# Kernel optimization log

Hardware: AMD Instinct MI355X
Metric: run time of the kernel (lower is better)

The kernel has to match this reference:

```python
import jax, jax.numpy as jnp
import numpy as np

B, T, C, H = 4, 2048, 1024, 16  # batch, seq, embed, heads; head_dim = C // H = 64


def setup_inputs() -> dict:
    key = jax.random.key(0)
    ks = jax.random.split(key, 9)
    s = 1.0 / np.sqrt(C)
    return {
        "query": jax.random.normal(ks[0], (B, T, C), jnp.float32),
        "key": jax.random.normal(ks[1], (B, T, C), jnp.float32),
        "value": jax.random.normal(ks[2], (B, T, C), jnp.float32),
        "mask": jax.random.randint(ks[3], (1, 1, T, T), 0, 2, jnp.int32),
        "Wq": jax.random.normal(ks[4], (C, C), jnp.float32) * s,
        "Wk": jax.random.normal(ks[5], (C, C), jnp.float32) * s,
        "Wv": jax.random.normal(ks[6], (C, C), jnp.float32) * s,
        "Wp": jax.random.normal(ks[7], (C, C), jnp.float32) * s,
        "bp": jax.random.normal(ks[8], (C,), jnp.float32) * s,
    }


def reference(query, key, value, mask, Wq, Wk, Wv, Wp, bp):
    # torch Linear: y = x @ W.T (no bias for q/k/v)
    q = jnp.einsum("btc,dc->btd", query, Wq)
    k = jnp.einsum("btc,dc->btd", key, Wk)
    v = jnp.einsum("btc,dc->btd", value, Wv)
    hd = C // H
    # [B,T,C] -> [B,H,T,hd]
    q = q.reshape(B, T, H, hd).transpose(0, 2, 1, 3)
    k = k.reshape(B, T, H, hd).transpose(0, 2, 1, 3)
    v = v.reshape(B, T, H, hd).transpose(0, 2, 1, 3)
    # NOTE: scale uses FULL embed dim C (faithful to source), not head_dim.
    wei = jnp.einsum("bhqd,bhkd->bhqk", q, k) * (C ** -0.5)
    # Faithful quirk: masked positions are zero-filled (not -inf) BEFORE softmax.
    wei = jnp.where(mask == 0, jnp.zeros((), wei.dtype), wei)
    wei = jax.nn.softmax(wei, axis=-1)
    out = jnp.einsum("bhqk,bhkd->bhqd", wei, v)
    out = out.transpose(0, 2, 1, 3).reshape(B, T, C)
    # proj (dropout omitted: eval mode / p=0)
    return jnp.einsum("btc,dc->btd", out, Wp) + bp
```

## Files before the change

kernel.cpp:

```cpp
#include <hip/hip_runtime.h>
#include <hip/hip_bf16.h>
#include <cstdint>
#include <cstddef>

static constexpr int Bn = 4, Tn = 2048, Cn = 1024, Hn = 16, HD = 64;
static constexpr int Mn = Bn * Tn;
static constexpr float SCALE = 0.03125f;

typedef __attribute__((ext_vector_type(8))) short s16x8;
typedef __attribute__((ext_vector_type(4))) short s16x4;
typedef __attribute__((ext_vector_type(4))) float f32x4;
typedef __attribute__((ext_vector_type(2))) unsigned u32x2;

#define DEVFN __device__ __forceinline__

DEVFN unsigned short f2bf(float f) {
  union { float f; unsigned u; } v; v.f = f;
  unsigned r = v.u + 0x7fffu + ((v.u >> 16) & 1u);
  return (unsigned short)(r >> 16);
}

DEVFN void gload_lds16(const void* g, void* l) {
  __builtin_amdgcn_global_load_lds(
      (const __attribute__((address_space(1))) void*)g,
      (__attribute__((address_space(3))) void*)l, 16, 0, 0);
}

__global__ __launch_bounds__(256) void k_cvt(const float* __restrict__ in,
                                             unsigned short* __restrict__ out, int n4) {
  int i = blockIdx.x * 256 + threadIdx.x;
  if (i >= n4) return;
  float4 v = reinterpret_cast<const float4*>(in)[i];
  ushort4 o;
  o.x = f2bf(v.x); o.y = f2bf(v.y); o.z = f2bf(v.z); o.w = f2bf(v.w);
  reinterpret_cast<ushort4*>(out)[i] = o;
}

__global__ __launch_bounds__(256) void k_pack(const int* __restrict__ mask,
                                              unsigned* __restrict__ bits) {
  int i = blockIdx.x * 256 + threadIdx.x;
  unsigned long long b = __ballot(mask[i] != 0);
  int lane = threadIdx.x & 63;
  if (lane == 0)        bits[i >> 5] = (unsigned)b;
  else if (lane == 32)  bits[i >> 5] = (unsigned)(b >> 32);
}

template <bool F32OUT>
__global__ __launch_bounds__(256) void k_gemm(const unsigned short* __restrict__ A,
                                              const unsigned short* __restrict__ Bt,
                                              void* __restrict__ Cv,
                                              const float* __restrict__ bias,
                                              float oscale,
                                              int M, int N, int K) {
  __shared__ __align__(16) char As[128 * 64 * 2];
  __shared__ __align__(16) char Bs[128 * 64 * 2];
  const int tid = threadIdx.x, lane = tid & 63, wid = tid >> 6;
  const int l15 = lane & 15, lg = lane >> 4;
  const int wm = (wid >> 1) * 64, wn = (wid & 1) * 64;
  const int m0 = blockIdx.y * 128, n0 = blockIdx.x * 128;

  f32x4 acc[4][4];
#pragma unroll
  for (int i = 0; i < 4; ++i)
#pragma unroll
    for (int j = 0; j < 4; ++j) acc[i][j] = f32x4{0.f, 0.f, 0.f, 0.f};

  for (int k0 = 0; k0 < K; k0 += 64) {
#pragma unroll
    for (int it = 0; it < 4; ++it) {
      int chunk = it * 256 + tid;
      int row = chunk >> 3;
      int kg = (chunk & 7) ^ (row & 7);
      gload_lds16(A + (size_t)(m0 + row) * K + k0 + kg * 8,
                  As + (it * 256 + wid * 64) * 16);
      gload_lds16(Bt + (size_t)(n0 + row) * K + k0 + kg * 8,
                  Bs + (it * 256 + wid * 64) * 16);
    }
    __syncthreads();
#pragma unroll
    for (int kk = 0; kk < 64; kk += 32) {
      s16x8 a[4], b[4];
#pragma unroll
      for (int i = 0; i < 4; ++i) {
        int ra = wm + i * 16 + l15;
        a[i] = *(const s16x8*)(As + ra * 128 + (((kk + lg * 8) * 2) ^ ((ra & 7) << 4)));
        int rb = wn + i * 16 + l15;
        b[i] = *(const s16x8*)(Bs + rb * 128 + (((kk + lg * 8) * 2) ^ ((rb & 7) << 4)));
      }
#pragma unroll
      for (int i = 0; i < 4; ++i)
#pragma unroll
        for (int j = 0; j < 4; ++j)
          acc[i][j] = __builtin_amdgcn_mfma_f32_16x16x32_bf16(a[i], b[j], acc[i][j], 0, 0, 0);
    }
    __syncthreads();
  }
#pragma unroll
  for (int i = 0; i < 4; ++i)
#pragma unroll
    for (int j = 0; j < 4; ++j)
#pragma unroll
      for (int q = 0; q < 4; ++q) {
        int r = m0 + wm + i * 16 + lg * 4 + q;
        int c = n0 + wn + j * 16 + l15;
        float v = acc[i][j][q];
        if (F32OUT) ((float*)Cv)[(size_t)r * N + c] = v + bias[c];
        else        ((unsigned short*)Cv)[(size_t)r * N + c] = f2bf(v * oscale);
      }
}

__global__ __launch_bounds__(256) void k_attn(const unsigned short* __restrict__ Qg,
                                              const unsigned short* __restrict__ Kg,
                                              const unsigned short* __restrict__ Vg,
                                              const unsigned* __restrict__ mbits,
                                              unsigned short* __restrict__ Og) {
  __shared__ __align__(16) char QPs[128 * 128];
  __shared__ __align__(16) char Ks[64 * 128];
  __shared__ __align__(16) char Vts[64 * 128];
  __shared__ unsigned Mw[128 * 2];
  __shared__ float Ls[128];

  const int tid = threadIdx.x, lane = tid & 63, wid = tid >> 6;
  const int l15 = lane & 15, lg = lane >> 4;
  const int qt = blockIdx.x, bh = blockIdx.y;
  const int b = bh >> 4, h = bh & 15;
  const size_t rowbase = (size_t)b * Tn;
  const int cbase = h * 64;

  const int dp = lane & 31;
  const int g  = wid * 2 + (lane >> 5);
  const int qrm = tid >> 1, wmi = tid & 1;

#pragma unroll
  for (int it = 0; it < 4; ++it) {
    int chunk = it * 256 + tid;
    int row = chunk >> 3;
    int kg = (chunk & 7) ^ (row & 7);
    gload_lds16(Qg + (rowbase + qt * 128 + row) * Cn + cbase + kg * 8,
                QPs + (it * 256 + wid * 64) * 16);
  }
#pragma unroll
  for (int it = 0; it < 2; ++it) {
    int chunk = it * 256 + tid;
    int row = chunk >> 3;
    int kg = (chunk & 7) ^ (row & 7);
    gload_lds16(Kg + (rowbase + row) * Cn + cbase + kg * 8,
                Ks + (it * 256 + wid * 64) * 16);
  }
  unsigned w[8];
  {
    const unsigned* vsrc = (const unsigned*)(Vg + (rowbase + g * 8) * Cn + cbase) + dp;
#pragma unroll
    for (int j = 0; j < 8; ++j) w[j] = vsrc[(size_t)j * (Cn / 2)];
  }
  unsigned mreg = mbits[(size_t)(qt * 128 + qrm) * (Tn / 32) + wmi];
  __syncthreads();

  s16x8 qf[2][2];
#pragma unroll
  for (int m = 0; m < 2; ++m)
#pragma unroll
    for (int kh = 0; kh < 2; ++kh) {
      int ra = wid * 32 + m * 16 + l15;
      qf[m][kh] = *(const s16x8*)(QPs + ra * 128 + ((kh * 64 + lg * 16) ^ ((ra & 7) << 4)));
    }
  {
    union { unsigned u[4]; s16x8 v; } lo, hi;
#pragma unroll
    for (int j = 0; j < 4; ++j) {
      lo.u[j] = __builtin_amdgcn_perm(w[2 * j + 1], w[2 * j], 0x05040100u);
      hi.u[j] = __builtin_amdgcn_perm(w[2 * j + 1], w[2 * j], 0x07060302u);
    }
    int d0 = dp * 2, swv = (dp & 7) << 4;
    *(s16x8*)(Vts + d0 * 128 + ((g * 16) ^ swv)) = lo.v;
    *(s16x8*)(Vts + (d0 + 1) * 128 + ((g * 16) ^ swv)) = hi.v;
    Mw[qrm * 2 + wmi] = mreg;
  }

  f32x4 oacc[2][4];
#pragma unroll
  for (int m = 0; m < 2; ++m)
#pragma unroll
    for (int n = 0; n < 4; ++n) oacc[m][n] = f32x4{0.f, 0.f, 0.f, 0.f};
  float lsum[2] = {0.0f, 0.0f};

  char* Pw = QPs + wid * (32 * 128);

  for (int kt = 0; kt < Tn / 64; ++kt) {
    f32x4 sacc[4][2];
#pragma unroll
    for (int n = 0; n < 4; ++n)
#pragma unroll
      for (int m = 0; m < 2; ++m) sacc[n][m] = f32x4{0.f, 0.f, 0.f, 0.f};
#pragma unroll
    for (int kk = 0; kk < 64; kk += 32) {
      s16x8 kfr[4];
#pragma unroll
      for (int n = 0; n < 4; ++n) {
        int rb = n * 16 + l15;
        kfr[n] = *(const s16x8*)(Ks + rb * 128 + (((kk + lg * 8) * 2) ^ ((rb & 7) << 4)));
      }
#pragma unroll
      for (int n = 0; n < 4; ++n)
#pragma unroll
        for (int m = 0; m < 2; ++m)
          sacc[n][m] = __builtin_amdgcn_mfma_f32_16x16x32_bf16(kfr[n], qf[m][kk >> 5],
                                                               sacc[n][m], 0, 0, 0);
    }
    __syncthreads();

    {
      int ktn = (kt + 1) & (Tn / 64 - 1);
#pragma unroll
      for (int it = 0; it < 2; ++it) {
        int chunk = it * 256 + tid;
        int row = chunk >> 3;
        int kg = (chunk & 7) ^ (row & 7);
        gload_lds16(Kg + (rowbase + ktn * 64 + row) * Cn + cbase + kg * 8,
                    Ks + (it * 256 + wid * 64) * 16);
      }
      const unsigned* vsrc =
          (const unsigned*)(Vg + (rowbase + ktn * 64 + g * 8) * Cn + cbase) + dp;
#pragma unroll
      for (int j = 0; j < 8; ++j) w[j] = vsrc[(size_t)j * (Cn / 2)];
      mreg = mbits[(size_t)(qt * 128 + qrm) * (Tn / 32) + ktn * 2 + wmi];
    }

#pragma unroll
    for (int qi = 0; qi < 2; ++qi) {
      int qr = wid * 32 + qi * 16 + l15;
      unsigned w0 = Mw[qr * 2], w1 = Mw[qr * 2 + 1];
      int qloc = qi * 16 + l15;
      unsigned swz = (unsigned)((qloc & 7) << 4);
      float psum = 0.0f;
#pragma unroll
      for (int kf = 0; kf < 4; ++kf) {
        unsigned wm_ = (kf < 2) ? w0 : w1;
        unsigned bits4 = wm_ >> ((kf & 1) * 16 + lg * 4);
        unsigned pb[4];
#pragma unroll
        for (int r = 0; r < 4; ++r) {
          int smear = (int)(bits4 << (31 - r)) >> 31;
          union { float f; unsigned u; } sv; sv.f = sacc[kf][qi][r];
          sv.u &= (unsigned)smear;
          float pv = __expf(sv.f);
          psum += pv;
          union { float f; unsigned u; } pc; pc.f = pv; pb[r] = pc.u;
        }
        union { u32x2 u; s16x4 s; } pk;
        pk.u.x = __builtin_amdgcn_perm(pb[1], pb[0], 0x07060302u);
        pk.u.y = __builtin_amdgcn_perm(pb[3], pb[2], 0x07060302u);
        *(s16x4*)(Pw + qloc * 128 + (((unsigned)(kf * 32 + lg * 8)) ^ swz)) = pk.s;
      }
      lsum[qi] += psum;
    }
    asm volatile("" ::: "memory");

#pragma unroll
    for (int kk = 0; kk < 64; kk += 32) {
      s16x8 pa[2], vb[4];
#pragma unroll
      for (int m = 0; m < 2; ++m) {
        int rp = m * 16 + l15;
        pa[m] = *(const s16x8*)(Pw + rp * 128 + (((kk + lg * 8) * 2) ^ ((rp & 7) << 4)));
      }
#pragma unroll
      for (int n = 0; n < 4; ++n) {
        int rv = n * 16 + l15;
        vb[n] = *(const s16x8*)(Vts + rv * 128 + (((kk + lg * 8) * 2) ^ (((rv >> 1) & 7) << 4)));
      }
#pragma unroll
      for (int m = 0; m < 2; ++m)
#pragma unroll
        for (int n = 0; n < 4; ++n)
          oacc[m][n] = __builtin_amdgcn_mfma_f32_16x16x32_bf16(pa[m], vb[n], oacc[m][n], 0, 0, 0);
    }
    __syncthreads();

    {
      union { unsigned u[4]; s16x8 v; } lo, hi;
#pragma unroll
      for (int j = 0; j < 4; ++j) {
        lo.u[j] = __builtin_amdgcn_perm(w[2 * j + 1], w[2 * j], 0x05040100u);
        hi.u[j] = __builtin_amdgcn_perm(w[2 * j + 1], w[2 * j], 0x07060302u);
      }
      int d0 = dp * 2, swv = (dp & 7) << 4;
      *(s16x8*)(Vts + d0 * 128 + ((g * 16) ^ swv)) = lo.v;
      *(s16x8*)(Vts + (d0 + 1) * 128 + ((g * 16) ^ swv)) = hi.v;
      Mw[qrm * 2 + wmi] = mreg;
    }
  }

#pragma unroll
  for (int qi = 0; qi < 2; ++qi) {
    float v = lsum[qi];
    v += __shfl_xor(v, 16);
    v += __shfl_xor(v, 32);
    if (lg == 0) Ls[wid * 32 + qi * 16 + l15] = v;
  }
  asm volatile("" ::: "memory");

#pragma unroll
  for (int m = 0; m < 2; ++m)
#pragma unroll
    for (int q = 0; q < 4; ++q) {
      int rloc = wid * 32 + m * 16 + lg * 4 + q;
      float inv = 1.0f / Ls[rloc];
      int rg = qt * 128 + rloc;
#pragma unroll
      for (int n = 0; n < 4; ++n)
        Og[(rowbase + rg) * Cn + cbase + n * 16 + l15] = f2bf(oacc[m][n][q] * inv);
    }
}

extern "C" void kernel_launch(void* const* d_in, const int* in_sizes, int n_in,
                              void* d_out, int out_size, void* d_ws, size_t ws_size,
                              hipStream_t stream) {
  (void)in_sizes; (void)n_in; (void)out_size; (void)ws_size;
  const float* query = (const float*)d_in[0];
  const float* key_  = (const float*)d_in[1];
  const float* value = (const float*)d_in[2];
  const int*   mask  = (const int*)d_in[3];
  const float* Wq = (const float*)d_in[4];
  const float* Wk = (const float*)d_in[5];
  const float* Wv = (const float*)d_in[6];
  const float* Wp = (const float*)d_in[7];
  const float* bp = (const float*)d_in[8];

  char* ws = (char*)d_ws;
  const size_t SX = (size_t)Mn * Cn * 2;
  const size_t SW = (size_t)Cn * Cn * 2;
  unsigned short* Xq  = (unsigned short*)(ws);
  unsigned short* Xk  = (unsigned short*)(ws + SX);
  unsigned short* Xv  = (unsigned short*)(ws + 2 * SX);
  unsigned short* Wqb = (unsigned short*)(ws + 3 * SX);
  unsigned short* Wkb = (unsigned short*)(ws + 3 * SX + SW);
  unsigned short* Wvb = (unsigned short*)(ws + 3 * SX + 2 * SW);
  unsigned short* Wpb = (unsigned short*)(ws + 3 * SX + 3 * SW);
  unsigned short* Qb  = (unsigned short*)(ws + 3 * SX + 4 * SW);
  unsigned short* Kb  = (unsigned short*)(ws + 4 * SX + 4 * SW);
  unsigned short* Vb  = (unsigned short*)(ws + 5 * SX + 4 * SW);
  unsigned*       mb  = (unsigned*)(ws + 6 * SX + 4 * SW);
  unsigned short* AO  = Xq;

  const int nX4 = Mn * Cn / 4, nW4 = Cn * Cn / 4;
  k_cvt<<<dim3(nX4 / 256), dim3(256), 0, stream>>>(query, Xq, nX4);
  k_cvt<<<dim3(nX4 / 256), dim3(256), 0, stream>>>(key_,  Xk, nX4);
  k_cvt<<<dim3(nX4 / 256), dim3(256), 0, stream>>>(value, Xv, nX4);
  k_cvt<<<dim3(nW4 / 256), dim3(256), 0, stream>>>(Wq, Wqb, nW4);
  k_cvt<<<dim3(nW4 / 256), dim3(256), 0, stream>>>(Wk, Wkb, nW4);
  k_cvt<<<dim3(nW4 / 256), dim3(256), 0, stream>>>(Wv, Wvb, nW4);
  k_cvt<<<dim3(nW4 / 256), dim3(256), 0, stream>>>(Wp, Wpb, nW4);
  k_pack<<<dim3((Tn * Tn) / 256), dim3(256), 0, stream>>>(mask, mb);

  dim3 gg(Cn / 128, Mn / 128);
  k_gemm<false><<<gg, dim3(256), 0, stream>>>(Xq, Wqb, Qb, nullptr, SCALE, Mn, Cn, Cn);
  k_gemm<false><<<gg, dim3(256), 0, stream>>>(Xk, Wkb, Kb, nullptr, 1.0f, Mn, Cn, Cn);
  k_gemm<false><<<gg, dim3(256), 0, stream>>>(Xv, Wvb, Vb, nullptr, 1.0f, Mn, Cn, Cn);

  k_attn<<<dim3(Tn / 128, Bn * Hn), dim3(256), 0, stream>>>(Qb, Kb, Vb, mb, AO);

  k_gemm<true><<<gg, dim3(256), 0, stream>>>(AO, Wpb, d_out, bp, 1.0f, Mn, Cn, Cn);
}
```

Before: 266.2 us.

## Merge prep kernels, batch QKV GEMMs, swizzle block order, use exp2 softmax

Combines the seven conversion launches and the mask packing into a single prep kernel, and runs the three QKV projections as one launch over a z-dimension. GEMM and attention blocks are remapped with an XCD-style swizzle so neighbouring tiles land on the same chiplet and share L2. The log2(e) factor is folded into the Q scale so softmax can call exp2 directly instead of __expf. The aim is to cut launch overhead and tail effects and to improve cache locality. In exchange the prep kernel picks its branch from the block index, and zero-filled masked scores still give exp2(0)=1, which matches exp(0)=1.

```diff
diff --git a/kernel.cpp b/kernel.cpp
--- a/kernel.cpp
+++ b/kernel.cpp
@@ -6,6 +6,7 @@
 static constexpr int Bn = 4, Tn = 2048, Cn = 1024, Hn = 16, HD = 64;
 static constexpr int Mn = Bn * Tn;
 static constexpr float SCALE = 0.03125f;
+static constexpr float QSCALE = 0.03125f * 1.4426950408889634f;
 
 typedef __attribute__((ext_vector_type(8))) short s16x8;
 typedef __attribute__((ext_vector_type(4))) short s16x4;
@@ -26,38 +27,57 @@
       (__attribute__((address_space(3))) void*)l, 16, 0, 0);
 }
 
-__global__ __launch_bounds__(256) void k_cvt(const float* __restrict__ in,
-                                             unsigned short* __restrict__ out, int n4) {
-  int i = blockIdx.x * 256 + threadIdx.x;
-  if (i >= n4) return;
-  float4 v = reinterpret_cast<const float4*>(in)[i];
-  ushort4 o;
-  o.x = f2bf(v.x); o.y = f2bf(v.y); o.z = f2bf(v.z); o.w = f2bf(v.w);
-  reinterpret_cast<ushort4*>(out)[i] = o;
-}
-
-__global__ __launch_bounds__(256) void k_pack(const int* __restrict__ mask,
-                                              unsigned* __restrict__ bits) {
-  int i = blockIdx.x * 256 + threadIdx.x;
-  unsigned long long b = __ballot(mask[i] != 0);
-  int lane = threadIdx.x & 63;
-  if (lane == 0)        bits[i >> 5] = (unsigned)b;
-  else if (lane == 32)  bits[i >> 5] = (unsigned)(b >> 32);
+__global__ __launch_bounds__(256) void k_prep(
+    const float* __restrict__ q, const float* __restrict__ k, const float* __restrict__ v,
+    const float* __restrict__ wq, const float* __restrict__ wk,
+    const float* __restrict__ wv, const float* __restrict__ wp,
+    const int* __restrict__ mask,
+    unsigned short* __restrict__ Xq, unsigned short* __restrict__ Xk,
+    unsigned short* __restrict__ Xv,
+    unsigned short* __restrict__ Wqb, unsigned short* __restrict__ Wkb,
+    unsigned short* __restrict__ Wvb, unsigned short* __restrict__ Wpb,
+    unsigned* __restrict__ bits) {
+  const int NX = (Mn * Cn / 4) / 256;
+  const int NW = (Cn * Cn / 4) / 256;
+  int bid = blockIdx.x, tid = threadIdx.x;
+  if (bid < 3 * NX) {
+    const float* src = bid < NX ? q : (bid < 2 * NX ? k : v);
+    unsigned short* dst = bid < NX ? Xq : (bid < 2 * NX ? Xk : Xv);
+    int i = (bid & (NX - 1)) * 256 + tid;
+    float4 vv = reinterpret_cast<const float4*>(src)[i];
+    ushort4 o;
+    o.x = f2bf(vv.x); o.y = f2bf(vv.y); o.z = f2bf(vv.z); o.w = f2bf(vv.w);
+    reinterpret_cast<ushort4*>(dst)[i] = o;
+  } else if (bid < 3 * NX + 4 * NW) {
+    int t = (bid - 3 * NX) / NW;
+    const float* src = t == 0 ? wq : t == 1 ? wk : t == 2 ? wv : wp;
+    unsigned short* dst = t == 0 ? Wqb : t == 1 ? Wkb : t == 2 ? Wvb : Wpb;
+    int i = ((bid - 3 * NX) & (NW - 1)) * 256 + tid;
+    float4 vv = reinterpret_cast<const float4*>(src)[i];
+    ushort4 o;
+    o.x = f2bf(vv.x); o.y = f2bf(vv.y); o.z = f2bf(vv.z); o.w = f2bf(vv.w);
+    reinterpret_cast<ushort4*>(dst)[i] = o;
+  } else {
+    int i = (bid - 3 * NX - 4 * NW) * 256 + tid;
+    unsigned long long b = __ballot(mask[i] != 0);
+    int lane = tid & 63;
+    if (lane == 0)        bits[i >> 5] = (unsigned)b;
+    else if (lane == 32)  bits[i >> 5] = (unsigned)(b >> 32);
+  }
 }
 
 template <bool F32OUT>
-__global__ __launch_bounds__(256) void k_gemm(const unsigned short* __restrict__ A,
-                                              const unsigned short* __restrict__ Bt,
-                                              void* __restrict__ Cv,
-                                              const float* __restrict__ bias,
-                                              float oscale,
-                                              int M, int N, int K) {
+DEVFN void gemm_body(const unsigned short* __restrict__ A,
+                     const unsigned short* __restrict__ Bt,
+                     void* __restrict__ Cv, const float* __restrict__ bias,
+                     float oscale, int bx, int by) {
+  const int M = Mn, N = Cn, K = Cn; (void)M;
   __shared__ __align__(16) char As[128 * 64 * 2];
   __shared__ __align__(16) char Bs[128 * 64 * 2];
   const int tid = threadIdx.x, lane = tid & 63, wid = tid >> 6;
   const int l15 = lane & 15, lg = lane >> 4;
   const int wm = (wid >> 1) * 64, wn = (wid & 1) * 64;
-  const int m0 = blockIdx.y * 128, n0 = blockIdx.x * 128;
+  const int m0 = by * 128, n0 = bx * 128;
 
   f32x4 acc[4][4];
 #pragma unroll
@@ -107,6 +127,36 @@
         if (F32OUT) ((float*)Cv)[(size_t)r * N + c] = v + bias[c];
         else        ((unsigned short*)Cv)[(size_t)r * N + c] = f2bf(v * oscale);
       }
+}
+
+DEVFN void gemm_swz(int& bx, int& by) {
+  int flat = blockIdx.y * 8 + blockIdx.x;
+  int swz = (flat & 7) * 64 + (flat >> 3);
+  bx = swz & 7; by = swz >> 3;
+}
+
+__global__ __launch_bounds__(256) void k_gemmQKV(
+    const unsigned short* __restrict__ Xq, const unsigned short* __restrict__ Xk,
+    const unsigned short* __restrict__ Xv,
+    const unsigned short* __restrict__ Wqb, const unsigned short* __restrict__ Wkb,
+    const unsigned short* __restrict__ Wvb,
+    unsigned short* __restrict__ Qb, unsigned short* __restrict__ Kb,
+    unsigned short* __restrict__ Vb) {
+  int z = blockIdx.z;
+  const unsigned short* A  = z == 0 ? Xq : z == 1 ? Xk : Xv;
+  const unsigned short* Bt = z == 0 ? Wqb : z == 1 ? Wkb : Wvb;
+  unsigned short* C        = z == 0 ? Qb : z == 1 ? Kb : Vb;
+  float oscale             = z == 0 ? QSCALE : 1.0f;
+  int bx, by; gemm_swz(bx, by);
+  gemm_body<false>(A, Bt, C, nullptr, oscale, bx, by);
+}
+
+__global__ __launch_bounds__(256) void k_gemmO(const unsigned short* __restrict__ A,
+                                               const unsigned short* __restrict__ Bt,
+                                               float* __restrict__ C,
+                                               const float* __restrict__ bias) {
+  int bx, by; gemm_swz(bx, by);
+  gemm_body<true>(A, Bt, C, bias, 1.0f, bx, by);
 }
 
 __global__ __launch_bounds__(256) void k_attn(const unsigned short* __restrict__ Qg,
@@ -122,7 +172,9 @@
 
   const int tid = threadIdx.x, lane = tid & 63, wid = tid >> 6;
   const int l15 = lane & 15, lg = lane >> 4;
-  const int qt = blockIdx.x, bh = blockIdx.y;
+  int flat = blockIdx.y * 16 + blockIdx.x;
+  int swz = (flat & 7) * 128 + (flat >> 3);
+  const int qt = swz & 15, bh = swz >> 4;
   const int b = bh >> 4, h = bh & 15;
   const size_t rowbase = (size_t)b * Tn;
   const int cbase = h * 64;
@@ -231,7 +283,7 @@
       int qr = wid * 32 + qi * 16 + l15;
       unsigned w0 = Mw[qr * 2], w1 = Mw[qr * 2 + 1];
       int qloc = qi * 16 + l15;
-      unsigned swz = (unsigned)((qloc & 7) << 4);
+      unsigned swp = (unsigned)((qloc & 7) << 4);
       float psum = 0.0f;
 #pragma unroll
       for (int kf = 0; kf < 4; ++kf) {
@@ -243,14 +295,14 @@
           int smear = (int)(bits4 << (31 - r)) >> 31;
           union { float f; unsigned u; } sv; sv.f = sacc[kf][qi][r];
           sv.u &= (unsigned)smear;
-          float pv = __expf(sv.f);
+          float pv = __builtin_exp2f(sv.f);
           psum += pv;
           union { float f; unsigned u; } pc; pc.f = pv; pb[r] = pc.u;
         }
         union { u32x2 u; s16x4 s; } pk;
         pk.u.x = __builtin_amdgcn_perm(pb[1], pb[0], 0x07060302u);
         pk.u.y = __builtin_amdgcn_perm(pb[3], pb[2], 0x07060302u);
-        *(s16x4*)(Pw + qloc * 128 + (((unsigned)(kf * 32 + lg * 8)) ^ swz)) = pk.s;
+        *(s16x4*)(Pw + qloc * 128 + (((unsigned)(kf * 32 + lg * 8)) ^ swp)) = pk.s;
       }
       lsum[qi] += psum;
     }
@@ -343,22 +395,15 @@
   unsigned*       mb  = (unsigned*)(ws + 6 * SX + 4 * SW);
   unsigned short* AO  = Xq;
 
-  const int nX4 = Mn * Cn / 4, nW4 = Cn * Cn / 4;
-  k_cvt<<<dim3(nX4 / 256), dim3(256), 0, stream>>>(query, Xq, nX4);
-  k_cvt<<<dim3(nX4 / 256), dim3(256), 0, stream>>>(key_,  Xk, nX4);
-  k_cvt<<<dim3(nX4 / 256), dim3(256), 0, stream>>>(value, Xv, nX4);
-  k_cvt<<<dim3(nW4 / 256), dim3(256), 0, stream>>>(Wq, Wqb, nW4);
-  k_cvt<<<dim3(nW4 / 256), dim3(256), 0, stream>>>(Wk, Wkb, nW4);
-  k_cvt<<<dim3(nW4 / 256), dim3(256), 0, stream>>>(Wv, Wvb, nW4);
-  k_cvt<<<dim3(nW4 / 256), dim3(256), 0, stream>>>(Wp, Wpb, nW4);
-  k_pack<<<dim3((Tn * Tn) / 256), dim3(256), 0, stream>>>(mask, mb);
-
-  dim3 gg(Cn / 128, Mn / 128);
-  k_gemm<false><<<gg, dim3(256), 0, stream>>>(Xq, Wqb, Qb, nullptr, SCALE, Mn, Cn, Cn);
-  k_gemm<false><<<gg, dim3(256), 0, stream>>>(Xk, Wkb, Kb, nullptr, 1.0f, Mn, Cn, Cn);
-  k_gemm<false><<<gg, dim3(256), 0, stream>>>(Xv, Wvb, Vb, nullptr, 1.0f, Mn, Cn, Cn);
-
-  k_attn<<<dim3(Tn / 128, Bn * Hn), dim3(256), 0, stream>>>(Qb, Kb, Vb, mb, AO);
-
-  k_gemm<true><<<gg, dim3(256), 0, stream>>>(AO, Wpb, d_out, bp, 1.0f, Mn, Cn, Cn);
-}
+  const int NPREP = 3 * ((Mn * Cn / 4) / 256) + 4 * ((Cn * Cn / 4) / 256)
+                    + (Tn * Tn) / 256;
+  k_prep<<<dim3(NPREP), dim3(256), 0, stream>>>(query, key_, value, Wq, Wk, Wv, Wp, mask,
+                                                Xq, Xk, Xv, Wqb, Wkb, Wvb, Wpb, mb);
+
+  k_gemmQKV<<<dim3(8, 64, 3), dim3(256), 0, stream>>>(Xq, Xk, Xv, Wqb, Wkb, Wvb,
+                                                      Qb, Kb, Vb);
+
+  k_attn<<<dim3(16, 64), dim3(256), 0, stream>>>(Qb, Kb, Vb, mb, AO);
+
+  k_gemmO<<<dim3(8, 64), dim3(256), 0, stream>>>(AO, Wpb, (float*)d_out, bp);
+}
```

After: 264.8 us. Within noise of the previous version (-0.5%).
